# Optimization experiments

Hardware: AMD Instinct MI355X
Metric: run time of the kernel (lower is better)

The kernel has to match this reference:

```python
import jax, jax.numpy as jnp
import numpy as np

TEMPERATURE = 0.1
EPS = 1e-12  # torch F.normalize eps

N, H, NUM_CLASSES = 8192, 1024, 64


def setup_inputs() -> dict:
    key = jax.random.key(0)
    k1, k2 = jax.random.split(key)
    utter_emb = jax.random.normal(k1, (N, H), dtype=jnp.float32)
    labels = jax.random.randint(k2, (N,), 0, NUM_CLASSES, dtype=jnp.int64)
    return {"utter_emb": utter_emb, "labels": labels}


def reference(utter_emb, labels):
    # Normalize rows -> cosine similarity matrix. (normalize + cosine_similarity
    # of already-normalized vectors == plain cosine sim of raw vectors.)
    norms = jnp.maximum(jnp.linalg.norm(utter_emb, axis=1, keepdims=True), EPS)
    x = utter_emb / norms                              # (N, H)
    sim = x @ x.T                                      # (N, N) cosine sims
    e = jnp.exp(sim / TEMPERATURE)                     # (N, N)

    n = utter_emb.shape[0]
    not_self = ~jnp.eye(n, dtype=bool)                 # exclude i itself
    pos_mask = (labels[:, None] == labels[None, :]) & not_self

    pos_cnt = pos_mask.sum(axis=1)                     # (N,)
    # numerator: mean over positives of exp(sim/T)
    numerator = (e * pos_mask).sum(axis=1) / jnp.maximum(pos_cnt, 1)
    # denominator: sum over ALL j != i (original neg_keys includes positives)
    denominator = (e * not_self).sum(axis=1)

    per_sample = -(jnp.log(numerator) - jnp.log(denominator))
    valid = pos_cnt > 0                                # only samples with >=1 positive
    count = valid.sum()
    cl_loss = jnp.where(valid, per_sample, 0.0).sum() / count
    return cl_loss
```

## Files before the change

### kernel.cpp

```cpp
#include <hip/hip_runtime.h>
#include <hip/hip_bf16.h>

#define N_ROWS 8192
#define H_DIM  1024
#define NUM_CLS 64
#define BM 128
#define BN 128
#define NBLK (N_ROWS / BM)
#define KSTRIDE ((size_t)N_ROWS * 16)
#define SCALE_E8M0 0x79797979
#define FIX2 1048576.0f
#define FIXSCALE 16777216.0
#define GRID_K2 (8 * 264)
#define NFIN 32

typedef float f32x4 __attribute__((ext_vector_type(4)));
typedef int   i32x4 __attribute__((ext_vector_type(4)));
typedef int   i32x8 __attribute__((ext_vector_type(8)));
typedef unsigned long long u64;

__device__ __forceinline__ float fast_exp2(float x) {
    float r;
    asm("v_exp_f32 %0, %1" : "=v"(r) : "v"(x));
    return r;
}

__device__ __forceinline__ unsigned enc_fp4(float f) {
    const float a = fabsf(f);
    unsigned c = (unsigned)(a > 0.25f) + (unsigned)(a > 0.75f) +
                 (unsigned)(a > 1.25f) + (unsigned)(a > 1.75f) +
                 (unsigned)(a > 2.5f)  + (unsigned)(a > 3.5f) +
                 (unsigned)(a > 5.0f);
    return c | ((__float_as_uint(f) >> 31) << 3);
}

__global__ __launch_bounds__(256) void norm_kernel(const float* __restrict__ in,
                                                   unsigned char* __restrict__ xqT,
                                                   u64* __restrict__ rsum_pos,
                                                   u64* __restrict__ rsum_all,
                                                   u64* __restrict__ acc) {
    if (blockIdx.x == 0 && threadIdx.x < 4) acc[threadIdx.x] = 0ULL;
    if (threadIdx.x < 16) {
        const int r0 = blockIdx.x * 16 + threadIdx.x;
        rsum_pos[r0] = 0ULL;
        rsum_all[r0] = 0ULL;
    }
    __shared__ __align__(16) unsigned char lt[16 * 528];
    const int tid  = threadIdx.x;
    const int wid  = tid >> 6, lane = tid & 63;
    const int r = lane >> 4, c = lane & 15;
    const int lrow = wid * 4 + r;
    const int row  = blockIdx.x * 16 + lrow;
    const float4* src = reinterpret_cast<const float4*>(in + (size_t)row * H_DIM)
                        + c * 16;
    float4 v[16];
    float ss = 0.f;
#pragma unroll
    for (int i = 0; i < 16; ++i) {
        v[i] = src[i];
        ss += v[i].x * v[i].x + v[i].y * v[i].y + v[i].z * v[i].z + v[i].w * v[i].w;
    }
#pragma unroll
    for (int d = 1; d < 16; d <<= 1) ss += __shfl_xor(ss, d, 64);
    const float inv = 64.0f / fmaxf(sqrtf(ss), 1e-12f);
#pragma unroll
    for (int h = 0; h < 2; ++h) {
        i32x4 dw;
#pragma unroll
        for (int j = 0; j < 4; ++j) {
            unsigned d = 0;
#pragma unroll
            for (int k = 0; k < 8; ++k) {
                const int e = j * 8 + k;
                const float f = ((const float*)&v[h * 8 + (e >> 2)])[e & 3] * inv;
                d |= enc_fp4(f) << (4 * k);
            }
            dw[j] = (int)d;
        }
        *reinterpret_cast<i32x4*>(&lt[lrow * 528 + (2 * c + h) * 16]) = dw;
    }
    __syncthreads();
#pragma unroll
    for (int it = 0; it < 2; ++it) {
        const int p  = it * 16 + (tid >> 4);
        const int rr = tid & 15;
        *reinterpret_cast<i32x4*>(xqT + (size_t)p * KSTRIDE +
                                  (size_t)(blockIdx.x * 16 + rr) * 16) =
            *reinterpret_cast<const i32x4*>(&lt[rr * 528 + p * 16]);
    }
}

__device__ __constant__ unsigned char OFF_TBL[28] = {
    1, 2, 3, 4, 5, 6, 7,
    10, 11, 12, 13, 14, 15,
    19, 20, 21, 22, 23,
    28, 29, 30, 31,
    37, 38, 39,
    46, 47,
    55
};

__global__ __launch_bounds__(256)
void simloss_kernel(const unsigned char* __restrict__ xqT, const int* __restrict__ labels,
                    u64* __restrict__ rsum_pos, u64* __restrict__ rsum_all) {
    __shared__ float sc[1024];

    const int xcd = blockIdx.x & 7;
    const int n   = blockIdx.x >> 3;
    int I, J;
    if (xcd < 4) {
        if (n >= 256) return;
        const int t = OFF_TBL[xcd * 4 + (n >> 6)];
        I = (t >> 3) * 8 + ((n >> 3) & 7);
        J = (t & 7) * 8 + (n & 7);
    } else if (n < 192) {
        const int t = OFF_TBL[16 + (xcd - 4) * 3 + (n >> 6)];
        I = (t >> 3) * 8 + ((n >> 3) & 7);
        J = (t & 7) * 8 + (n & 7);
    } else {
        int n2 = n - 192;
        const int D = (xcd - 4) * 2 + (n2 >= 36 ? 1 : 0);
        int t2 = (n2 >= 36) ? n2 - 36 : n2;
        int i = 0;
        while (t2 >= 8 - i) { t2 -= 8 - i; ++i; }
        I = D * 8 + i;
        J = D * 8 + i + t2;
    }
    const bool diag = (I == J);
    const int row0 = I * BM, col0 = J * BN;

    const int tid  = threadIdx.x;
    const int lane = tid & 63;
    const int wid  = tid >> 6;
    const int wr = wid >> 1, wc = wid & 1;
    const int l15 = lane & 15, lq = lane >> 4;

    f32x4 acc[4][4];
#pragma unroll
    for (int m = 0; m < 4; ++m)
#pragma unroll
        for (int n2 = 0; n2 < 4; ++n2) acc[m][n2] = (f32x4){0.f, 0.f, 0.f, 0.f};

    const unsigned char* Ap = xqT + (size_t)lq * KSTRIDE + (size_t)(row0 + wr * 64 + l15) * 16;
    const unsigned char* Bp = xqT + (size_t)lq * KSTRIDE + (size_t)(col0 + wc * 64 + l15) * 16;

#define LOADS(BUF, S)                                                          \
    do {                                                                       \
        _Pragma("unroll")                                                      \
        for (int m = 0; m < 4; ++m)                                            \
            A##BUF[m] = *reinterpret_cast<const i32x4*>(                       \
                Ap + (size_t)(S) * 4 * KSTRIDE + m * 256);                     \
        _Pragma("unroll")                                                      \
        for (int n2 = 0; n2 < 4; ++n2)                                         \
            B##BUF[n2] = *reinterpret_cast<const i32x4*>(                      \
                Bp + (size_t)(S) * 4 * KSTRIDE + n2 * 256);                    \
    } while (0)

#define BUILD8(dst, src) (dst) = __builtin_shufflevector((src), (src),         \
                                                         0, 1, 2, 3, -1, -1, -1, -1)

#define STEP(CUR, NXT, S, LAST)                                                \
    do {                                                                       \
        if (!(LAST)) LOADS(NXT, (S) + 1);                                      \
        i32x8 b80, b81, b82, b83;                                              \
        BUILD8(b80, B##CUR[0]); BUILD8(b81, B##CUR[1]);                        \
        BUILD8(b82, B##CUR[2]); BUILD8(b83, B##CUR[3]);                        \
        __builtin_amdgcn_s_setprio(1);                                         \
        _Pragma("unroll")                                                      \
        for (int m = 0; m < 4; ++m) {                                          \
            i32x8 a8;                                                          \
            BUILD8(a8, A##CUR[m]);                                             \
            acc[m][0] = __builtin_amdgcn_mfma_scale_f32_16x16x128_f8f6f4(      \
                a8, b80, acc[m][0], 4, 4, 0, SCALE_E8M0, 0, SCALE_E8M0);       \
            acc[m][1] = __builtin_amdgcn_mfma_scale_f32_16x16x128_f8f6f4(      \
                a8, b81, acc[m][1], 4, 4, 0, SCALE_E8M0, 0, SCALE_E8M0);       \
            acc[m][2] = __builtin_amdgcn_mfma_scale_f32_16x16x128_f8f6f4(      \
                a8, b82, acc[m][2], 4, 4, 0, SCALE_E8M0, 0, SCALE_E8M0);       \
            acc[m][3] = __builtin_amdgcn_mfma_scale_f32_16x16x128_f8f6f4(      \
                a8, b83, acc[m][3], 4, 4, 0, SCALE_E8M0, 0, SCALE_E8M0);       \
        }                                                                      \
        __builtin_amdgcn_s_setprio(0);                                         \
    } while (0)

    i32x4 A0[4], B0[4], A1[4], B1[4];
    LOADS(0, 0);
    STEP(0, 1, 0, false);
    STEP(1, 0, 1, false);
    STEP(0, 1, 2, false);
    STEP(1, 0, 3, false);
    STEP(0, 1, 4, false);
    STEP(1, 0, 5, false);
    STEP(0, 1, 6, false);
    STEP(1, 0, 7, true);
#undef LOADS
#undef BUILD8
#undef STEP

    int lab_r[16];
#pragma unroll
    for (int m = 0; m < 4; ++m)
#pragma unroll
        for (int r = 0; r < 4; ++r)
            lab_r[m * 4 + r] = labels[row0 + wr * 64 + m * 16 + lq * 4 + r];

    float rs_pos[16], rs_all[16];
#pragma unroll
    for (int i = 0; i < 16; ++i) { rs_pos[i] = 0.f; rs_all[i] = 0.f; }
    float cs_pos[4], cs_all[4];
#pragma unroll
    for (int n2 = 0; n2 < 4; ++n2) { cs_pos[n2] = 0.f; cs_all[n2] = 0.f; }

#pragma unroll
    for (int n2 = 0; n2 < 4; ++n2) {
        const int colg = col0 + wc * 64 + n2 * 16 + l15;
        const int lab_c = labels[colg];
#pragma unroll
        for (int m = 0; m < 4; ++m) {
#pragma unroll
            for (int r = 0; r < 4; ++r) {
                const int rowg = row0 + wr * 64 + m * 16 + lq * 4 + r;
                const float e = fast_exp2(acc[m][n2][r] * 14.4269504088896340736f);
                const bool self = (rowg == colg);
                const bool pos  = (lab_c == lab_r[m * 4 + r]) && !self;
                const float ea = self ? 0.f : e;
                const float ep = pos ? e : 0.f;
                rs_all[m * 4 + r] += ea;
                rs_pos[m * 4 + r] += ep;
                cs_all[n2] += ea;
                cs_pos[n2] += ep;
            }
        }
    }

#pragma unroll
    for (int i = 0; i < 16; ++i) {
#pragma unroll
        for (int d = 1; d < 16; d <<= 1) {
            rs_pos[i] += __shfl_xor(rs_pos[i], d, 64);
            rs_all[i] += __shfl_xor(rs_all[i], d, 64);
        }
    }
#pragma unroll
    for (int n2 = 0; n2 < 4; ++n2) {
#pragma unroll
        for (int d = 16; d < 64; d <<= 1) {
            cs_pos[n2] += __shfl_xor(cs_pos[n2], d, 64);
            cs_all[n2] += __shfl_xor(cs_all[n2], d, 64);
        }
    }

    float* rowpos = sc;
    float* rowall = sc + 256;
    float* colpos = sc + 512;
    float* colall = sc + 768;
    if (l15 == 0) {
#pragma unroll
        for (int i = 0; i < 16; ++i) {
            const int m = i >> 2, r = i & 3;
            const int lr = wr * 64 + m * 16 + lq * 4 + r;
            rowpos[wc * 128 + lr] = rs_pos[i];
            rowall[wc * 128 + lr] = rs_all[i];
        }
    }
    if (lq == 0 && !diag) {
#pragma unroll
        for (int n2 = 0; n2 < 4; ++n2) {
            const int lc = wc * 64 + n2 * 16 + l15;
            colpos[wr * 128 + lc] = cs_pos[n2];
            colall[wr * 128 + lc] = cs_all[n2];
        }
    }
    __syncthreads();

    if (tid < 128) {
        const float rp = rowpos[tid] + rowpos[128 + tid];
        const float ra = rowall[tid] + rowall[128 + tid];
        atomicAdd(&rsum_pos[row0 + tid], (u64)(rp * FIX2 + 0.5f));
        atomicAdd(&rsum_all[row0 + tid], (u64)(ra * FIX2 + 0.5f));
    } else if (!diag) {
        const int t2 = tid - 128;
        const float cp = colpos[t2] + colpos[128 + t2];
        const float ca = colall[t2] + colall[128 + t2];
        atomicAdd(&rsum_pos[col0 + t2], (u64)(cp * FIX2 + 0.5f));
        atomicAdd(&rsum_all[col0 + t2], (u64)(ca * FIX2 + 0.5f));
    }
}

__global__ __launch_bounds__(256)
void finalize_kernel(const int* __restrict__ labels, const u64* __restrict__ rsum_pos,
                     const u64* __restrict__ rsum_all, u64* __restrict__ acc,
                     float* __restrict__ out) {
    __shared__ int hist[NUM_CLS];
    __shared__ float sred[4];
    __shared__ int scnt[4];
    const int tid = threadIdx.x;
    if (tid < NUM_CLS) hist[tid] = 0;
    __syncthreads();
    for (int i = tid; i < N_ROWS; i += 256) atomicAdd(&hist[labels[i]], 1);
    __syncthreads();

    const int i = blockIdx.x * 256 + tid;
    const u64 rp = rsum_pos[i];
    const u64 ra = rsum_all[i];
    const int cnt = hist[labels[i]] - 1;
    float lsum = 0.f;
    int vcnt = 0;
    if (cnt > 0) {
        const float p = fmaxf((float)((double)rp / (double)FIX2), 1e-30f);
        const float a = (float)((double)ra / (double)FIX2);
        lsum = logf(a) - logf(p) + logf((float)cnt);
        vcnt = 1;
    }
    const int lane = tid & 63, wid = tid >> 6;
#pragma unroll
    for (int d = 1; d < 64; d <<= 1) {
        lsum += __shfl_xor(lsum, d, 64);
        vcnt += __shfl_xor(vcnt, d, 64);
    }
    if (lane == 0) { sred[wid] = lsum; scnt[wid] = vcnt; }
    __syncthreads();
    if (tid == 0) {
        const double bs = (double)(sred[0] + sred[1] + sred[2] + sred[3]);
        const u64 S = (u64)(bs * FIXSCALE + 0.5);
        const u64 C = (u64)(scnt[0] + scnt[1] + scnt[2] + scnt[3]);
        atomicAdd(&acc[1], S);
        atomicAdd(&acc[2], C);
        __threadfence();
        const u64 tk = atomicAdd(&acc[0], 1ULL);
        if (tk == (u64)(NFIN - 1)) {
            volatile u64* va = acc;
            const double St = (double)va[1];
            const double Ct = (double)va[2];
            out[0] = (float)(St / FIXSCALE / Ct);
        }
    }
}

extern "C" void kernel_launch(void* const* d_in, const int* in_sizes, int n_in,
                              void* d_out, int out_size, void* d_ws, size_t ws_size,
                              hipStream_t stream) {
    const float* emb   = (const float*)d_in[0];
    const int* labels  = (const int*)d_in[1];
    float* out         = (float*)d_out;
    char* ws           = (char*)d_ws;

    unsigned char* xqT = (unsigned char*)ws;
    u64* rsum_pos = (u64*)(ws + (size_t)32 * KSTRIDE);
    u64* rsum_all = rsum_pos + N_ROWS;
    u64* acc      = rsum_all + N_ROWS;

    norm_kernel<<<N_ROWS / 16, 256, 0, stream>>>(emb, xqT, rsum_pos, rsum_all, acc);
    simloss_kernel<<<GRID_K2, 256, 0, stream>>>(xqT, labels, rsum_pos, rsum_all);
    finalize_kernel<<<NFIN, 256, 0, stream>>>(labels, rsum_pos, rsum_all, acc, out);
}
```

Before: 64.62 us.

## Enlarge similarity tiles to 256x256 with 512-thread blocks over upper-triangle pairs

Replaces the 128x128 tile schedule and its XCD-aware lookup table with 256x256 tiles over the upper-triangular tile pairs, computed by 8 waves per block, each handling a 64x128 sub-tile. Larger tiles raise arithmetic intensity per loaded fp4 fragment and halve the number of global atomics per element of output. In exchange each wave uses twice as many accumulator and B-fragment registers, which may cut occupancy. The grid drops to 528 blocks, which may leave the GPU underfilled, and the simple block-to-tile mapping loses the previous XCD locality scheme.

```diff
diff --git a/kernel.cpp b/kernel.cpp
--- a/kernel.cpp
+++ b/kernel.cpp
@@ -4,14 +4,13 @@
 #define N_ROWS 8192
 #define H_DIM  1024
 #define NUM_CLS 64
-#define BM 128
-#define BN 128
-#define NBLK (N_ROWS / BM)
+#define BT 256
+#define NP (N_ROWS / BT)
+#define NPAIR (NP * (NP + 1) / 2)
 #define KSTRIDE ((size_t)N_ROWS * 16)
 #define SCALE_E8M0 0x79797979
 #define FIX2 1048576.0f
 #define FIXSCALE 16777216.0
-#define GRID_K2 (8 * 264)
 #define NFIN 32
 
 typedef float f32x4 __attribute__((ext_vector_type(4)));
@@ -90,59 +89,33 @@
     }
 }
 
-__device__ __constant__ unsigned char OFF_TBL[28] = {
-    1, 2, 3, 4, 5, 6, 7,
-    10, 11, 12, 13, 14, 15,
-    19, 20, 21, 22, 23,
-    28, 29, 30, 31,
-    37, 38, 39,
-    46, 47,
-    55
-};
-
-__global__ __launch_bounds__(256)
+__global__ __launch_bounds__(512, 2)
 void simloss_kernel(const unsigned char* __restrict__ xqT, const int* __restrict__ labels,
                     u64* __restrict__ rsum_pos, u64* __restrict__ rsum_all) {
-    __shared__ float sc[1024];
-
-    const int xcd = blockIdx.x & 7;
-    const int n   = blockIdx.x >> 3;
-    int I, J;
-    if (xcd < 4) {
-        if (n >= 256) return;
-        const int t = OFF_TBL[xcd * 4 + (n >> 6)];
-        I = (t >> 3) * 8 + ((n >> 3) & 7);
-        J = (t & 7) * 8 + (n & 7);
-    } else if (n < 192) {
-        const int t = OFF_TBL[16 + (xcd - 4) * 3 + (n >> 6)];
-        I = (t >> 3) * 8 + ((n >> 3) & 7);
-        J = (t & 7) * 8 + (n & 7);
-    } else {
-        int n2 = n - 192;
-        const int D = (xcd - 4) * 2 + (n2 >= 36 ? 1 : 0);
-        int t2 = (n2 >= 36) ? n2 - 36 : n2;
-        int i = 0;
-        while (t2 >= 8 - i) { t2 -= 8 - i; ++i; }
-        I = D * 8 + i;
-        J = D * 8 + i + t2;
-    }
+    __shared__ float sc[3072];
+
+    const int bid = (blockIdx.x & 7) * (NPAIR / 8) + (blockIdx.x >> 3);
+    int t = bid, I = 0;
+    while (t >= NP - I) { t -= NP - I; ++I; }
+    const int J = I + t;
     const bool diag = (I == J);
-    const int row0 = I * BM, col0 = J * BN;
+    const int row0 = I * BT, col0 = J * BT;
 
     const int tid  = threadIdx.x;
     const int lane = tid & 63;
     const int wid  = tid >> 6;
-    const int wr = wid >> 1, wc = wid & 1;
+    const int wm = wid >> 1;
+    const int wn = wid & 1;
     const int l15 = lane & 15, lq = lane >> 4;
 
-    f32x4 acc[4][4];
+    f32x4 acc[4][8];
 #pragma unroll
     for (int m = 0; m < 4; ++m)
 #pragma unroll
-        for (int n2 = 0; n2 < 4; ++n2) acc[m][n2] = (f32x4){0.f, 0.f, 0.f, 0.f};
-
-    const unsigned char* Ap = xqT + (size_t)lq * KSTRIDE + (size_t)(row0 + wr * 64 + l15) * 16;
-    const unsigned char* Bp = xqT + (size_t)lq * KSTRIDE + (size_t)(col0 + wc * 64 + l15) * 16;
+        for (int n2 = 0; n2 < 8; ++n2) acc[m][n2] = (f32x4){0.f, 0.f, 0.f, 0.f};
+
+    const unsigned char* Ap = xqT + (size_t)lq * KSTRIDE + (size_t)(row0 + wm * 64 + l15) * 16;
+    const unsigned char* Bp = xqT + (size_t)lq * KSTRIDE + (size_t)(col0 + wn * 128 + l15) * 16;
 
 #define LOADS(BUF, S)                                                          \
     do {                                                                       \
@@ -151,7 +124,7 @@
             A##BUF[m] = *reinterpret_cast<const i32x4*>(                       \
                 Ap + (size_t)(S) * 4 * KSTRIDE + m * 256);                     \
         _Pragma("unroll")                                                      \
-        for (int n2 = 0; n2 < 4; ++n2)                                         \
+        for (int n2 = 0; n2 < 8; ++n2)                                         \
             B##BUF[n2] = *reinterpret_cast<const i32x4*>(                      \
                 Bp + (size_t)(S) * 4 * KSTRIDE + n2 * 256);                    \
     } while (0)
@@ -162,27 +135,23 @@
 #define STEP(CUR, NXT, S, LAST)                                                \
     do {                                                                       \
         if (!(LAST)) LOADS(NXT, (S) + 1);                                      \
-        i32x8 b80, b81, b82, b83;                                              \
-        BUILD8(b80, B##CUR[0]); BUILD8(b81, B##CUR[1]);                        \
-        BUILD8(b82, B##CUR[2]); BUILD8(b83, B##CUR[3]);                        \
+        i32x8 b8[8];                                                           \
+        _Pragma("unroll")                                                      \
+        for (int n2 = 0; n2 < 8; ++n2) BUILD8(b8[n2], B##CUR[n2]);             \
         __builtin_amdgcn_s_setprio(1);                                         \
         _Pragma("unroll")                                                      \
         for (int m = 0; m < 4; ++m) {                                          \
             i32x8 a8;                                                          \
             BUILD8(a8, A##CUR[m]);                                             \
-            acc[m][0] = __builtin_amdgcn_mfma_scale_f32_16x16x128_f8f6f4(      \
-                a8, b80, acc[m][0], 4, 4, 0, SCALE_E8M0, 0, SCALE_E8M0);       \
-            acc[m][1] = __builtin_amdgcn_mfma_scale_f32_16x16x128_f8f6f4(      \
-                a8, b81, acc[m][1], 4, 4, 0, SCALE_E8M0, 0, SCALE_E8M0);       \
-            acc[m][2] = __builtin_amdgcn_mfma_scale_f32_16x16x128_f8f6f4(      \
-                a8, b82, acc[m][2], 4, 4, 0, SCALE_E8M0, 0, SCALE_E8M0);       \
-            acc[m][3] = __builtin_amdgcn_mfma_scale_f32_16x16x128_f8f6f4(      \
-                a8, b83, acc[m][3], 4, 4, 0, SCALE_E8M0, 0, SCALE_E8M0);       \
+            _Pragma("unroll")                                                  \
+            for (int n2 = 0; n2 < 8; ++n2)                                     \
+                acc[m][n2] = __builtin_amdgcn_mfma_scale_f32_16x16x128_f8f6f4( \
+                    a8, b8[n2], acc[m][n2], 4, 4, 0, SCALE_E8M0, 0, SCALE_E8M0); \
         }                                                                      \
         __builtin_amdgcn_s_setprio(0);                                         \
     } while (0)
 
-    i32x4 A0[4], B0[4], A1[4], B1[4];
+    i32x4 A0[4], B0[8], A1[4], B1[8];
     LOADS(0, 0);
     STEP(0, 1, 0, false);
     STEP(1, 0, 1, false);
@@ -201,24 +170,24 @@
     for (int m = 0; m < 4; ++m)
 #pragma unroll
         for (int r = 0; r < 4; ++r)
-            lab_r[m * 4 + r] = labels[row0 + wr * 64 + m * 16 + lq * 4 + r];
+            lab_r[m * 4 + r] = labels[row0 + wm * 64 + m * 16 + lq * 4 + r];
 
     float rs_pos[16], rs_all[16];
 #pragma unroll
     for (int i = 0; i < 16; ++i) { rs_pos[i] = 0.f; rs_all[i] = 0.f; }
-    float cs_pos[4], cs_all[4];
-#pragma unroll
-    for (int n2 = 0; n2 < 4; ++n2) { cs_pos[n2] = 0.f; cs_all[n2] = 0.f; }
-
-#pragma unroll
-    for (int n2 = 0; n2 < 4; ++n2) {
-        const int colg = col0 + wc * 64 + n2 * 16 + l15;
+    float cs_pos[8], cs_all[8];
+#pragma unroll
+    for (int n2 = 0; n2 < 8; ++n2) { cs_pos[n2] = 0.f; cs_all[n2] = 0.f; }
+
+#pragma unroll
+    for (int n2 = 0; n2 < 8; ++n2) {
+        const int colg = col0 + wn * 128 + n2 * 16 + l15;
         const int lab_c = labels[colg];
 #pragma unroll
         for (int m = 0; m < 4; ++m) {
 #pragma unroll
             for (int r = 0; r < 4; ++r) {
-                const int rowg = row0 + wr * 64 + m * 16 + lq * 4 + r;
+                const int rowg = row0 + wm * 64 + m * 16 + lq * 4 + r;
                 const float e = fast_exp2(acc[m][n2][r] * 14.4269504088896340736f);
                 const bool self = (rowg == colg);
                 const bool pos  = (lab_c == lab_r[m * 4 + r]) && !self;
@@ -241,7 +210,7 @@
         }
     }
 #pragma unroll
-    for (int n2 = 0; n2 < 4; ++n2) {
+    for (int n2 = 0; n2 < 8; ++n2) {
 #pragma unroll
         for (int d = 16; d < 64; d <<= 1) {
             cs_pos[n2] += __shfl_xor(cs_pos[n2], d, 64);
@@ -250,39 +219,39 @@
     }
 
     float* rowpos = sc;
-    float* rowall = sc + 256;
-    float* colpos = sc + 512;
-    float* colall = sc + 768;
+    float* rowall = sc + 512;
+    float* colpos = sc + 1024;
+    float* colall = sc + 2048;
     if (l15 == 0) {
 #pragma unroll
         for (int i = 0; i < 16; ++i) {
             const int m = i >> 2, r = i & 3;
-            const int lr = wr * 64 + m * 16 + lq * 4 + r;
-            rowpos[wc * 128 + lr] = rs_pos[i];
-            rowall[wc * 128 + lr] = rs_all[i];
+            const int lr = wm * 64 + m * 16 + lq * 4 + r;
+            rowpos[wn * 256 + lr] = rs_pos[i];
+            rowall[wn * 256 + lr] = rs_all[i];
         }
     }
     if (lq == 0 && !diag) {
 #pragma unroll
-        for (int n2 = 0; n2 < 4; ++n2) {
-            const int lc = wc * 64 + n2 * 16 + l15;
-            colpos[wr * 128 + lc] = cs_pos[n2];
-            colall[wr * 128 + lc] = cs_all[n2];
-        }
-    }
-    __syncthreads();
-
-    if (tid < 128) {
-        const float rp = rowpos[tid] + rowpos[128 + tid];
-        const float ra = rowall[tid] + rowall[128 + tid];
+        for (int n2 = 0; n2 < 8; ++n2) {
+            const int lc = wn * 128 + n2 * 16 + l15;
+            colpos[wm * 256 + lc] = cs_pos[n2];
+            colall[wm * 256 + lc] = cs_all[n2];
+        }
+    }
+    __syncthreads();
+
+    if (tid < 256) {
+        const float rp = rowpos[tid] + rowpos[256 + tid];
+        const float ra = rowall[tid] + rowall[256 + tid];
         atomicAdd(&rsum_pos[row0 + tid], (u64)(rp * FIX2 + 0.5f));
         atomicAdd(&rsum_all[row0 + tid], (u64)(ra * FIX2 + 0.5f));
     } else if (!diag) {
-        const int t2 = tid - 128;
-        const float cp = colpos[t2] + colpos[128 + t2];
-        const float ca = colall[t2] + colall[128 + t2];
-        atomicAdd(&rsum_pos[col0 + t2], (u64)(cp * FIX2 + 0.5f));
-        atomicAdd(&rsum_all[col0 + t2], (u64)(ca * FIX2 + 0.5f));
+        const int c = tid - 256;
+        const float cp = colpos[c] + colpos[256 + c] + colpos[512 + c] + colpos[768 + c];
+        const float ca = colall[c] + colall[256 + c] + colall[512 + c] + colall[768 + c];
+        atomicAdd(&rsum_pos[col0 + c], (u64)(cp * FIX2 + 0.5f));
+        atomicAdd(&rsum_all[col0 + c], (u64)(ca * FIX2 + 0.5f));
     }
 }
 
@@ -350,6 +319,6 @@
     u64* acc      = rsum_all + N_ROWS;
 
     norm_kernel<<<N_ROWS / 16, 256, 0, stream>>>(emb, xqT, rsum_pos, rsum_all, acc);
-    simloss_kernel<<<GRID_K2, 256, 0, stream>>>(xqT, labels, rsum_pos, rsum_all);
+    simloss_kernel<<<NPAIR, 512, 0, stream>>>(xqT, labels, rsum_pos, rsum_all);
     finalize_kernel<<<NFIN, 256, 0, stream>>>(labels, rsum_pos, rsum_all, acc, out);
 }
```

After: 67.69 us. 4.7% more time.

## Fuse finalize into simloss via last-block ticket and simplify tile mapping

Applied to the files above, without the earlier changes.

Removes the separate finalize kernel launch: each simloss block increments a global ticket after its atomics, and the last block computes the class histogram and the loss reduction over all rows. The tile-to-block mapping is replaced by a simple triangular enumeration with an XCD-strided block id, which drops the hand-tuned offset table. This saves one launch and its gap, but it serialises the final reduction over 8192 rows onto a single block and may lose the previous XCD locality arrangement.

```diff
diff --git a/kernel.cpp b/kernel.cpp
--- a/kernel.cpp
+++ b/kernel.cpp
@@ -6,13 +6,11 @@
 #define NUM_CLS 64
 #define BM 128
 #define BN 128
-#define NBLK (N_ROWS / BM)
+#define NP (N_ROWS / BM)
+#define NPAIR (NP * (NP + 1) / 2)
 #define KSTRIDE ((size_t)N_ROWS * 16)
 #define SCALE_E8M0 0x79797979
 #define FIX2 1048576.0f
-#define FIXSCALE 16777216.0
-#define GRID_K2 (8 * 264)
-#define NFIN 32
 
 typedef float f32x4 __attribute__((ext_vector_type(4)));
 typedef int   i32x4 __attribute__((ext_vector_type(4)));
@@ -90,42 +88,17 @@
     }
 }
 
-__device__ __constant__ unsigned char OFF_TBL[28] = {
-    1, 2, 3, 4, 5, 6, 7,
-    10, 11, 12, 13, 14, 15,
-    19, 20, 21, 22, 23,
-    28, 29, 30, 31,
-    37, 38, 39,
-    46, 47,
-    55
-};
-
 __global__ __launch_bounds__(256)
 void simloss_kernel(const unsigned char* __restrict__ xqT, const int* __restrict__ labels,
-                    u64* __restrict__ rsum_pos, u64* __restrict__ rsum_all) {
+                    u64* __restrict__ rsum_pos, u64* __restrict__ rsum_all,
+                    u64* __restrict__ acc, float* __restrict__ out) {
     __shared__ float sc[1024];
-
-    const int xcd = blockIdx.x & 7;
-    const int n   = blockIdx.x >> 3;
-    int I, J;
-    if (xcd < 4) {
-        if (n >= 256) return;
-        const int t = OFF_TBL[xcd * 4 + (n >> 6)];
-        I = (t >> 3) * 8 + ((n >> 3) & 7);
-        J = (t & 7) * 8 + (n & 7);
-    } else if (n < 192) {
-        const int t = OFF_TBL[16 + (xcd - 4) * 3 + (n >> 6)];
-        I = (t >> 3) * 8 + ((n >> 3) & 7);
-        J = (t & 7) * 8 + (n & 7);
-    } else {
-        int n2 = n - 192;
-        const int D = (xcd - 4) * 2 + (n2 >= 36 ? 1 : 0);
-        int t2 = (n2 >= 36) ? n2 - 36 : n2;
-        int i = 0;
-        while (t2 >= 8 - i) { t2 -= 8 - i; ++i; }
-        I = D * 8 + i;
-        J = D * 8 + i + t2;
-    }
+    __shared__ int tkflag;
+
+    const int bid = (blockIdx.x & 7) * (NPAIR / 8) + (blockIdx.x >> 3);
+    int t = bid, I = 0;
+    while (t >= NP - I) { t -= NP - I; ++I; }
+    const int J = I + t;
     const bool diag = (I == J);
     const int row0 = I * BM, col0 = J * BN;
 
@@ -135,11 +108,11 @@
     const int wr = wid >> 1, wc = wid & 1;
     const int l15 = lane & 15, lq = lane >> 4;
 
-    f32x4 acc[4][4];
+    f32x4 acc4[4][4];
 #pragma unroll
     for (int m = 0; m < 4; ++m)
 #pragma unroll
-        for (int n2 = 0; n2 < 4; ++n2) acc[m][n2] = (f32x4){0.f, 0.f, 0.f, 0.f};
+        for (int n2 = 0; n2 < 4; ++n2) acc4[m][n2] = (f32x4){0.f, 0.f, 0.f, 0.f};
 
     const unsigned char* Ap = xqT + (size_t)lq * KSTRIDE + (size_t)(row0 + wr * 64 + l15) * 16;
     const unsigned char* Bp = xqT + (size_t)lq * KSTRIDE + (size_t)(col0 + wc * 64 + l15) * 16;
@@ -170,14 +143,14 @@
         for (int m = 0; m < 4; ++m) {                                          \
             i32x8 a8;                                                          \
             BUILD8(a8, A##CUR[m]);                                             \
-            acc[m][0] = __builtin_amdgcn_mfma_scale_f32_16x16x128_f8f6f4(      \
-                a8, b80, acc[m][0], 4, 4, 0, SCALE_E8M0, 0, SCALE_E8M0);       \
-            acc[m][1] = __builtin_amdgcn_mfma_scale_f32_16x16x128_f8f6f4(      \
-                a8, b81, acc[m][1], 4, 4, 0, SCALE_E8M0, 0, SCALE_E8M0);       \
-            acc[m][2] = __builtin_amdgcn_mfma_scale_f32_16x16x128_f8f6f4(      \
-                a8, b82, acc[m][2], 4, 4, 0, SCALE_E8M0, 0, SCALE_E8M0);       \
-            acc[m][3] = __builtin_amdgcn_mfma_scale_f32_16x16x128_f8f6f4(      \
-                a8, b83, acc[m][3], 4, 4, 0, SCALE_E8M0, 0, SCALE_E8M0);       \
+            acc4[m][0] = __builtin_amdgcn_mfma_scale_f32_16x16x128_f8f6f4(     \
+                a8, b80, acc4[m][0], 4, 4, 0, SCALE_E8M0, 0, SCALE_E8M0);      \
+            acc4[m][1] = __builtin_amdgcn_mfma_scale_f32_16x16x128_f8f6f4(     \
+                a8, b81, acc4[m][1], 4, 4, 0, SCALE_E8M0, 0, SCALE_E8M0);      \
+            acc4[m][2] = __builtin_amdgcn_mfma_scale_f32_16x16x128_f8f6f4(     \
+                a8, b82, acc4[m][2], 4, 4, 0, SCALE_E8M0, 0, SCALE_E8M0);      \
+            acc4[m][3] = __builtin_amdgcn_mfma_scale_f32_16x16x128_f8f6f4(     \
+                a8, b83, acc4[m][3], 4, 4, 0, SCALE_E8M0, 0, SCALE_E8M0);      \
         }                                                                      \
         __builtin_amdgcn_s_setprio(0);                                         \
     } while (0)
@@ -219,7 +192,7 @@
 #pragma unroll
             for (int r = 0; r < 4; ++r) {
                 const int rowg = row0 + wr * 64 + m * 16 + lq * 4 + r;
-                const float e = fast_exp2(acc[m][n2][r] * 14.4269504088896340736f);
+                const float e = fast_exp2(acc4[m][n2][r] * 14.4269504088896340736f);
                 const bool self = (rowg == colg);
                 const bool pos  = (lab_c == lab_r[m * 4 + r]) && !self;
                 const float ea = self ? 0.f : e;
@@ -284,55 +257,51 @@
         atomicAdd(&rsum_pos[col0 + t2], (u64)(cp * FIX2 + 0.5f));
         atomicAdd(&rsum_all[col0 + t2], (u64)(ca * FIX2 + 0.5f));
     }
-}
-
-__global__ __launch_bounds__(256)
-void finalize_kernel(const int* __restrict__ labels, const u64* __restrict__ rsum_pos,
-                     const u64* __restrict__ rsum_all, u64* __restrict__ acc,
-                     float* __restrict__ out) {
+
+    __threadfence();
+    __syncthreads();
+    if (tid == 0) {
+        const u64 tk = atomicAdd(&acc[0], 1ULL);
+        tkflag = (tk == (u64)(NPAIR - 1)) ? 1 : 0;
+    }
+    __syncthreads();
+    if (!tkflag) return;
+
     __shared__ int hist[NUM_CLS];
     __shared__ float sred[4];
     __shared__ int scnt[4];
-    const int tid = threadIdx.x;
     if (tid < NUM_CLS) hist[tid] = 0;
     __syncthreads();
     for (int i = tid; i < N_ROWS; i += 256) atomicAdd(&hist[labels[i]], 1);
     __syncthreads();
 
-    const int i = blockIdx.x * 256 + tid;
-    const u64 rp = rsum_pos[i];
-    const u64 ra = rsum_all[i];
-    const int cnt = hist[labels[i]] - 1;
     float lsum = 0.f;
     int vcnt = 0;
-    if (cnt > 0) {
-        const float p = fmaxf((float)((double)rp / (double)FIX2), 1e-30f);
-        const float a = (float)((double)ra / (double)FIX2);
-        lsum = logf(a) - logf(p) + logf((float)cnt);
-        vcnt = 1;
-    }
-    const int lane = tid & 63, wid = tid >> 6;
+    for (int k = 0; k < N_ROWS / 256; ++k) {
+        const int i = k * 256 + tid;
+        const u64 rp = __hip_atomic_load(&rsum_pos[i], __ATOMIC_RELAXED,
+                                         __HIP_MEMORY_SCOPE_AGENT);
+        const u64 ra = __hip_atomic_load(&rsum_all[i], __ATOMIC_RELAXED,
+                                         __HIP_MEMORY_SCOPE_AGENT);
+        const int cnt = hist[labels[i]] - 1;
+        if (cnt > 0) {
+            const float p = fmaxf((float)((double)rp / (double)FIX2), 1e-30f);
+            const float a = (float)((double)ra / (double)FIX2);
+            lsum += logf(a) - logf(p) + logf((float)cnt);
+            vcnt += 1;
+        }
+    }
 #pragma unroll
     for (int d = 1; d < 64; d <<= 1) {
         lsum += __shfl_xor(lsum, d, 64);
         vcnt += __shfl_xor(vcnt, d, 64);
     }
-    if (lane == 0) { sred[wid] = lsum; scnt[wid] = vcnt; }
+    if ((tid & 63) == 0) { sred[tid >> 6] = lsum; scnt[tid >> 6] = vcnt; }
     __syncthreads();
     if (tid == 0) {
-        const double bs = (double)(sred[0] + sred[1] + sred[2] + sred[3]);
-        const u64 S = (u64)(bs * FIXSCALE + 0.5);
-        const u64 C = (u64)(scnt[0] + scnt[1] + scnt[2] + scnt[3]);
-        atomicAdd(&acc[1], S);
-        atomicAdd(&acc[2], C);
-        __threadfence();
-        const u64 tk = atomicAdd(&acc[0], 1ULL);
-        if (tk == (u64)(NFIN - 1)) {
-            volatile u64* va = acc;
-            const double St = (double)va[1];
-            const double Ct = (double)va[2];
-            out[0] = (float)(St / FIXSCALE / Ct);
-        }
+        const double S = (double)(sred[0] + sred[1] + sred[2] + sred[3]);
+        const double C = (double)(scnt[0] + scnt[1] + scnt[2] + scnt[3]);
+        out[0] = (float)(S / C);
     }
 }
 
@@ -350,6 +319,5 @@
     u64* acc      = rsum_all + N_ROWS;
 
     norm_kernel<<<N_ROWS / 16, 256, 0, stream>>>(emb, xqT, rsum_pos, rsum_all, acc);
-    simloss_kernel<<<GRID_K2, 256, 0, stream>>>(xqT, labels, rsum_pos, rsum_all);
-    finalize_kernel<<<NFIN, 256, 0, stream>>>(labels, rsum_pos, rsum_all, acc, out);
-}
+    simloss_kernel<<<NPAIR, 256, 0, stream>>>(xqT, labels, rsum_pos, rsum_all, acc, out);
+}
```

Result: slower. 188.9 us (+192.3%).
